# Kernel optimization log

Hardware: AMD Instinct MI355X
Metric: run time of the kernel (lower is better)

Reference implementation:

```python
import jax, jax.numpy as jnp
import numpy as np

SP_BETA = 1.0       # rendering_options.sp_beta
INF_DELTA = 1e10    # use_inf_depth=True -> last delta is 1e10
EPS = 1e-10


def setup_inputs() -> dict:
    key = jax.random.key(0)
    k1, k2, k3 = jax.random.split(key, 3)
    B, R, S, C = 8, 16384, 64, 3  # batch, rays, samples-per-ray, rgb channels
    colors = jax.random.normal(k1, (B, R, S, C), dtype=jnp.float32)
    densities = jax.random.normal(k2, (B, R, S, 1), dtype=jnp.float32)
    # depths must be sorted (increasing) along the sample dimension
    depths = jnp.sort(
        jax.random.uniform(k3, (B, R, S, 1), dtype=jnp.float32, minval=0.1, maxval=6.0),
        axis=2,
    )
    return {"colors": colors, "densities": densities, "depths": depths}


def reference(colors, densities, depths):
    # deltas between consecutive samples, last delta = 1e10 (infinite far plane)
    deltas = depths[:, :, 1:] - depths[:, :, :-1]                      # [B,R,S-1,1]
    deltas = jnp.concatenate(
        [deltas, jnp.full_like(deltas[:, :, :1], INF_DELTA)], axis=2)  # [B,R,S,1]

    # clamp_mode == 'softplus' with beta=1.0: softplus(x*beta)/beta
    dens = jax.nn.softplus(densities * SP_BETA) / SP_BETA              # [B,R,S,1]

    alphas = 1.0 - jnp.exp(-deltas * dens)                             # [B,R,S,1]

    # transmittance: cumulative product of (1-alpha), with leading ones
    trans = jnp.cumprod(1.0 - alphas + EPS, axis=2)                    # [B,R,S,1]
    trans = jnp.concatenate([jnp.ones_like(trans[:, :, :1]), trans], axis=2)  # [B,R,S+1,1]

    final_transmittance = trans[:, :, -1, 0]                           # [B,R]
    weights = alphas * trans[:, :, :-1]                                # [B,R,S,1]

    rgb_final = (weights * colors).sum(axis=2)                         # [B,R,C]
    depth = (weights * depths).sum(axis=2)                             # [B,R,1]
    return rgb_final, depth, weights, final_transmittance
```

## Files before the change

kernel.cpp:

```cpp
#include <hip/hip_runtime.h>

#define INF_DELTA 1e10f
#define LOG2E 1.4426950408889634f
#define LOG2_EPS -33.219280948873623f

template<int CTRL, int RMASK>
__device__ __forceinline__ float dpp0(float v) {
    return __int_as_float(
        __builtin_amdgcn_update_dpp(0, __float_as_int(v), CTRL, RMASK, 0xF, false));
}

__device__ __forceinline__ float wave_incl_scan_add(float v) {
    v += dpp0<0x111, 0xF>(v);
    v += dpp0<0x112, 0xF>(v);
    v += dpp0<0x114, 0xF>(v);
    v += dpp0<0x118, 0xF>(v);
    v += dpp0<0x142, 0xA>(v);
    v += dpp0<0x143, 0xC>(v);
    return v;
}

__global__ __launch_bounds__(256) void raymarch_kernel(
    const float* __restrict__ colors,
    const float* __restrict__ densities,
    const float* __restrict__ depths,
    float* __restrict__ rgb_out,
    float* __restrict__ depth_out,
    float* __restrict__ weights_out,
    float* __restrict__ trans_out,
    int n_rays)
{
    const int lane = threadIdx.x & 63;
    const int ray  = blockIdx.x * 4 + (threadIdx.x >> 6);
    if (ray >= n_rays) return;

    const long base = (long)ray * 64 + lane;

    const float d      = depths[base];
    const float d_next = depths[base + ((lane < 63) ? 1 : 0)];
    const float x      = densities[base];
    const float3 c     = *reinterpret_cast<const float3*>(colors + (long)ray * 192 + lane * 3);

    const float delta = (lane == 63) ? INF_DELTA : (d_next - d);

    const float q   = __builtin_amdgcn_exp2f(-__builtin_fabsf(x) * LOG2E);
    const float l2  = __builtin_amdgcn_logf(1.0f + q);
    const float sp2 = __builtin_fmaf(__builtin_fmaxf(x, 0.0f), LOG2E, l2);
    const float g   = -delta * sp2;
    const float y   = __builtin_amdgcn_exp2f(g);
    const float alpha = 1.0f - y;

    const float llane = __builtin_fmaxf(g, LOG2_EPS);

    const float S          = wave_incl_scan_add(llane);
    const float trans_excl = __builtin_amdgcn_exp2f(S - llane);

    const float w = alpha * trans_excl;
    weights_out[base] = w;

    float s0 = w * c.x, s1 = w * c.y, s2 = w * c.z, s3 = w * d;
    s0 += dpp0<0xB1, 0xF>(s0);
    s1 += dpp0<0xB1, 0xF>(s1);
    s2 += dpp0<0xB1, 0xF>(s2);
    s3 += dpp0<0xB1, 0xF>(s3);
    s0 += dpp0<0x4E, 0xF>(s0);
    s1 += dpp0<0x4E, 0xF>(s1);
    s2 += dpp0<0x4E, 0xF>(s2);
    s3 += dpp0<0x4E, 0xF>(s3);

    const int sel = lane & 3;
    float v = (sel == 0) ? s0 : (sel == 1) ? s1 : (sel == 2) ? s2 : s3;
    v += dpp0<0x124, 0xF>(v);
    v += dpp0<0x128, 0xF>(v);
    v += __int_as_float(__builtin_amdgcn_ds_swizzle(__float_as_int(v), 0x401F));
    v += __shfl_xor(v, 32, 64);

    if (lane < 3) {
        rgb_out[(long)ray * 3 + lane] = v;
    } else if (lane == 3) {
        depth_out[ray] = v;
    } else if (lane == 63) {
        trans_out[ray] = __builtin_amdgcn_exp2f(S);
    }
}

extern "C" void kernel_launch(void* const* d_in, const int* in_sizes, int n_in,
                              void* d_out, int out_size, void* d_ws, size_t ws_size,
                              hipStream_t stream) {
    const float* colors    = (const float*)d_in[0];
    const float* densities = (const float*)d_in[1];
    const float* depths    = (const float*)d_in[2];

    const int n_rays = in_sizes[1] / 64;

    float* out      = (float*)d_out;
    float* rgb      = out;
    float* depth_o  = rgb + (long)n_rays * 3;
    float* weights  = depth_o + n_rays;
    float* trans    = weights + (long)n_rays * 64;

    const int blocks = (n_rays + 3) / 4;
    raymarch_kernel<<<blocks, 256, 0, stream>>>(
        colors, densities, depths, rgb, depth_o, weights, trans, n_rays);
}
```

Baseline: 198.8 us.

## Process four samples per lane with vector loads and a 16-lane scan per ray

Each wave now handles four rays, with each lane owning four consecutive samples. Depths, densities and colors are read with float4 loads, and weights are written with float4 stores. The transmittance scan does a serial prefix over the four samples and then a 16-lane DPP scan, so the cross-row DPP steps, ds_swizzle and shfl_xor are gone. The aim is fewer, wider memory transactions and less cross-lane work per sample. In exchange each lane does more serial work and holds more registers, and the launch assumes the ray count is a multiple of four.

```diff
diff --git a/kernel.cpp b/kernel.cpp
--- a/kernel.cpp
+++ b/kernel.cpp
@@ -10,14 +10,10 @@
         __builtin_amdgcn_update_dpp(0, __float_as_int(v), CTRL, RMASK, 0xF, false));
 }
 
-__device__ __forceinline__ float wave_incl_scan_add(float v) {
-    v += dpp0<0x111, 0xF>(v);
-    v += dpp0<0x112, 0xF>(v);
-    v += dpp0<0x114, 0xF>(v);
-    v += dpp0<0x118, 0xF>(v);
-    v += dpp0<0x142, 0xA>(v);
-    v += dpp0<0x143, 0xC>(v);
-    return v;
+__device__ __forceinline__ float log2_softplus(float x) {
+    const float q  = __builtin_amdgcn_exp2f(-__builtin_fabsf(x) * LOG2E);
+    const float l2 = __builtin_amdgcn_logf(1.0f + q);
+    return __builtin_fmaf(__builtin_fmaxf(x, 0.0f), LOG2E, l2);
 }
 
 __global__ __launch_bounds__(256) void raymarch_kernel(
@@ -31,56 +27,91 @@
     int n_rays)
 {
     const int lane = threadIdx.x & 63;
-    const int ray  = blockIdx.x * 4 + (threadIdx.x >> 6);
-    if (ray >= n_rays) return;
+    const int wid  = threadIdx.x >> 6;
+    const int blk  = blockIdx.x * 4 + wid;
+    const int nblk = n_rays >> 2;
+    if (blk >= nblk) return;
 
-    const long base = (long)ray * 64 + lane;
+    const long fbase = (long)blk * 256;
 
-    const float d      = depths[base];
-    const float d_next = depths[base + ((lane < 63) ? 1 : 0)];
-    const float x      = densities[base];
-    const float3 c     = *reinterpret_cast<const float3*>(colors + (long)ray * 192 + lane * 3);
+    const float4 d4 = *reinterpret_cast<const float4*>(depths    + fbase + lane * 4);
+    const float4 x4 = *reinterpret_cast<const float4*>(densities + fbase + lane * 4);
+    const float* cp = colors + fbase * 3 + lane * 12;
+    const float4 ca = *reinterpret_cast<const float4*>(cp);
+    const float4 cb = *reinterpret_cast<const float4*>(cp + 4);
+    const float4 cc = *reinterpret_cast<const float4*>(cp + 8);
 
-    const float delta = (lane == 63) ? INF_DELTA : (d_next - d);
+    const float dnx  = dpp0<0x101, 0xF>(d4.x);
+    const float del0 = d4.y - d4.x;
+    const float del1 = d4.z - d4.y;
+    const float del2 = d4.w - d4.z;
+    const float del3 = ((lane & 15) == 15) ? INF_DELTA : (dnx - d4.w);
 
-    const float q   = __builtin_amdgcn_exp2f(-__builtin_fabsf(x) * LOG2E);
-    const float l2  = __builtin_amdgcn_logf(1.0f + q);
-    const float sp2 = __builtin_fmaf(__builtin_fmaxf(x, 0.0f), LOG2E, l2);
-    const float g   = -delta * sp2;
-    const float y   = __builtin_amdgcn_exp2f(g);
-    const float alpha = 1.0f - y;
+    const float g0 = -del0 * log2_softplus(x4.x);
+    const float g1 = -del1 * log2_softplus(x4.y);
+    const float g2 = -del2 * log2_softplus(x4.z);
+    const float g3 = -del3 * log2_softplus(x4.w);
+    const float a0 = 1.0f - __builtin_amdgcn_exp2f(g0);
+    const float a1 = 1.0f - __builtin_amdgcn_exp2f(g1);
+    const float a2 = 1.0f - __builtin_amdgcn_exp2f(g2);
+    const float a3 = 1.0f - __builtin_amdgcn_exp2f(g3);
+    const float l0 = __builtin_fmaxf(g0, LOG2_EPS);
+    const float l1 = __builtin_fmaxf(g1, LOG2_EPS);
+    const float l2 = __builtin_fmaxf(g2, LOG2_EPS);
+    const float l3 = __builtin_fmaxf(g3, LOG2_EPS);
 
-    const float llane = __builtin_fmaxf(g, LOG2_EPS);
+    const float L0 = l0;
+    const float L1 = L0 + l1;
+    const float L2 = L1 + l2;
+    const float L3 = L2 + l3;
+    float p = L3;
+    p += dpp0<0x111, 0xF>(p);
+    p += dpp0<0x112, 0xF>(p);
+    p += dpp0<0x114, 0xF>(p);
+    p += dpp0<0x118, 0xF>(p);
+    const float excl = p - L3;
 
-    const float S          = wave_incl_scan_add(llane);
-    const float trans_excl = __builtin_amdgcn_exp2f(S - llane);
+    const float e0 = __builtin_amdgcn_exp2f(excl);
+    const float e1 = __builtin_amdgcn_exp2f(excl + L0);
+    const float e2 = __builtin_amdgcn_exp2f(excl + L1);
+    const float e3 = __builtin_amdgcn_exp2f(excl + L2);
 
-    const float w = alpha * trans_excl;
-    weights_out[base] = w;
+    const float w0 = a0 * e0;
+    const float w1 = a1 * e1;
+    const float w2 = a2 * e2;
+    const float w3 = a3 * e3;
 
-    float s0 = w * c.x, s1 = w * c.y, s2 = w * c.z, s3 = w * d;
-    s0 += dpp0<0xB1, 0xF>(s0);
-    s1 += dpp0<0xB1, 0xF>(s1);
-    s2 += dpp0<0xB1, 0xF>(s2);
-    s3 += dpp0<0xB1, 0xF>(s3);
-    s0 += dpp0<0x4E, 0xF>(s0);
-    s1 += dpp0<0x4E, 0xF>(s1);
-    s2 += dpp0<0x4E, 0xF>(s2);
-    s3 += dpp0<0x4E, 0xF>(s3);
+    float4 wv; wv.x = w0; wv.y = w1; wv.z = w2; wv.w = w3;
+    *reinterpret_cast<float4*>(weights_out + fbase + lane * 4) = wv;
 
+    float p0 = w0 * ca.x + w1 * ca.w + w2 * cb.z + w3 * cc.y;
+    float p1 = w0 * ca.y + w1 * cb.x + w2 * cb.w + w3 * cc.z;
+    float p2 = w0 * ca.z + w1 * cb.y + w2 * cc.x + w3 * cc.w;
+    float p3 = w0 * d4.x + w1 * d4.y + w2 * d4.z + w3 * d4.w;
+
+    p0 += dpp0<0xB1, 0xF>(p0);
+    p1 += dpp0<0xB1, 0xF>(p1);
+    p2 += dpp0<0xB1, 0xF>(p2);
+    p3 += dpp0<0xB1, 0xF>(p3);
+    p0 += dpp0<0x4E, 0xF>(p0);
+    p1 += dpp0<0x4E, 0xF>(p1);
+    p2 += dpp0<0x4E, 0xF>(p2);
+    p3 += dpp0<0x4E, 0xF>(p3);
+
+    const int c = lane & 15;
     const int sel = lane & 3;
-    float v = (sel == 0) ? s0 : (sel == 1) ? s1 : (sel == 2) ? s2 : s3;
+    float v = (sel == 0) ? p0 : (sel == 1) ? p1 : (sel == 2) ? p2 : p3;
     v += dpp0<0x124, 0xF>(v);
     v += dpp0<0x128, 0xF>(v);
-    v += __int_as_float(__builtin_amdgcn_ds_swizzle(__float_as_int(v), 0x401F));
-    v += __shfl_xor(v, 32, 64);
 
-    if (lane < 3) {
-        rgb_out[(long)ray * 3 + lane] = v;
-    } else if (lane == 3) {
+    const int ray = blk * 4 + (lane >> 4);
+    if (c < 3) {
+        rgb_out[(long)ray * 3 + c] = v;
+    } else if (c == 3) {
         depth_out[ray] = v;
-    } else if (lane == 63) {
-        trans_out[ray] = __builtin_amdgcn_exp2f(S);
+    }
+    if (c == 15) {
+        trans_out[ray] = __builtin_amdgcn_exp2f(p);
     }
 }
 
@@ -99,7 +130,8 @@
     float* weights  = depth_o + n_rays;
     float* trans    = weights + (long)n_rays * 64;
 
-    const int blocks = (n_rays + 3) / 4;
+    const int nblk   = n_rays / 4;
+    const int blocks = (nblk + 3) / 4;
     raymarch_kernel<<<blocks, 256, 0, stream>>>(
         colors, densities, depths, rgb, depth_o, weights, trans, n_rays);
 }
```

Result: no change. 201.3 us (+1.3%).
